# Kernel optimization log

Hardware: AMD Instinct MI355X
Metric: run time of the kernel (lower is better)

Reference implementation:

```python
import jax, jax.numpy as jnp
import numpy as np

IMG_W, IMG_H = 512, 512      # cfg.NETWORK.IMAGE_SIZE
HM_W, HM_H = 128, 128        # cfg.NETWORK.HEATMAP_SIZE
CUBE = (64, 64, 64)          # cube_size (voxel resolution)
N_VIEWS, BATCH, N_JOINTS = 5, 4, 15


def setup_inputs() -> dict:
    key = jax.random.key(0)
    k1, k2, k3 = jax.random.split(key, 3)
    heatmaps = jax.random.uniform(k1, (N_VIEWS, BATCH, N_JOINTS, HM_H, HM_W), jnp.float32)
    projM = jax.random.normal(k2, (N_VIEWS, BATCH, 3, 4), jnp.float32)
    grid_center = jax.random.normal(k3, (BATCH, 3), jnp.float32)
    return {"heatmaps": heatmaps, "projM": projM, "grid_center": grid_center, "grid_size": 8000}


def _compute_grid(grid_size, center):
    # torch.linspace(-s/2, s/2, n) + center[d], meshgrid 'ij' -> flattened [P, 3]
    half = jnp.float32(grid_size) * 0.5
    axes = [jnp.linspace(-half, half, n) + center[d] for d, n in enumerate(CUBE)]
    gx, gy, gz = jnp.meshgrid(*axes, indexing="ij")
    return jnp.stack([gx.ravel(), gy.ravel(), gz.ravel()], axis=-1)


def _bilinear(img, coords):
    # img: [J, H, W]; coords: [P, 2] normalized to [-1, 1], align_corners=True, zero padding
    J, H, W = img.shape
    ix = (coords[:, 0] + 1.0) * 0.5 * (W - 1)
    iy = (coords[:, 1] + 1.0) * 0.5 * (H - 1)
    x0 = jnp.floor(ix); y0 = jnp.floor(iy)
    x1 = x0 + 1.0;      y1 = y0 + 1.0
    wx1 = ix - x0; wx0 = 1.0 - wx1
    wy1 = iy - y0; wy0 = 1.0 - wy1

    def corner(xf, yf, w):
        valid = ((xf >= 0) & (xf <= W - 1) & (yf >= 0) & (yf <= H - 1)).astype(img.dtype)
        xi = jnp.clip(xf, 0, W - 1).astype(jnp.int32)
        yi = jnp.clip(yf, 0, H - 1).astype(jnp.int32)
        return img[:, yi, xi] * (w * valid)[None, :]  # [J, P]

    return (corner(x0, y0, wx0 * wy0) + corner(x1, y0, wx1 * wy0)
            + corner(x0, y1, wx0 * wy1) + corner(x1, y1, wx1 * wy1))


def reference(heatmaps, projM, grid_center, grid_size):
    n, B, J, H, W = heatmaps.shape
    dt = heatmaps.dtype
    # world-space voxel grids, one per batch sample: [B, P, 3]
    grids = jax.vmap(lambda c: _compute_grid(grid_size, c))(grid_center)
    P = grids.shape[1]
    # project_pose_sync takes grid with axes permuted [x, z, y]; pinhole 3x4 projection + perspective divide
    pts = grids[:, :, jnp.array([0, 2, 1])]
    homog = jnp.concatenate([pts, jnp.ones_like(pts[..., :1])], axis=-1)  # [B, P, 4]
    proj = jnp.einsum("nbij,bpj->nbpi", projM, homog)                     # [n, B, P, 3]
    xy = proj[..., :2] / proj[..., 2:3]                                   # [n, B, P, 2]
    # visibility mask per view
    inb = ((xy[..., 0] >= 0) & (xy[..., 1] >= 0)
           & (xy[..., 0] < IMG_W) & (xy[..., 1] < IMG_H)).astype(dt)      # [n, B, P]
    xy = jnp.clip(xy, -1.0, float(max(IMG_W, IMG_H)))
    xy = xy * jnp.array([HM_W / IMG_W, HM_H / IMG_H], dt)
    sg = jnp.clip(xy / jnp.array([HM_W - 1, HM_H - 1], dt) * 2.0 - 1.0, -1.1, 1.1)
    # bilinear grid_sample over all (view, batch) pairs at once
    samp = jax.vmap(_bilinear)(heatmaps.reshape(n * B, J, H, W),
                               sg.reshape(n * B, P, 2))                   # [n*B, J, P]
    samp = samp.reshape(n, B, J, P)
    num = jnp.einsum("nbjp,nbp->bjp", samp, inb)
    den = jnp.sum(inb, axis=0) + 1e-6                                     # [B, P]
    cubes = num / den[:, None, :]
    cubes = jnp.clip(jnp.where(jnp.isnan(cubes), 0.0, cubes), 0.0, 1.0)
    cubes = cubes.reshape(B, J, *CUBE)
    return cubes, grids
```

## Files before the change

### kernel.cpp

```cpp
#include <hip/hip_runtime.h>

#define NV 5
#define NB 4
#define NJ 15
#define HMW 128
#define HMH 128
#define P_TOTAL (64 * 64 * 64)
#define HM_PLANE (HMH * HMW)
#define CUBES_ELEMS ((size_t)NB * NJ * P_TOTAL)
#define N_PLANES (NV * NB * NJ)
#define QUAD_BYTES ((size_t)N_PLANES * HM_PLANE * 4)

typedef float f32x4 __attribute__((ext_vector_type(4)));
struct F2 { float x, y; };

__device__ __forceinline__ int dot4_i8(unsigned int a, unsigned int b, int c) {
#if __has_builtin(__builtin_amdgcn_sdot4)
    return __builtin_amdgcn_sdot4((int)a, (int)b, c, false);
#else
    return c + (int)(a & 0xff)         * (int)(b & 0xff)
             + (int)((a >> 8) & 0xff)  * (int)((b >> 8) & 0xff)
             + (int)((a >> 16) & 0xff) * (int)((b >> 16) & 0xff)
             + (int)((a >> 24) & 0xff) * (int)((b >> 24) & 0xff);
#endif
}

__global__ __launch_bounds__(256) void build_quads_i8(
    const float* __restrict__ hm, unsigned int* __restrict__ q)
{
    const int idx = blockIdx.x * 256 + threadIdx.x;
    const int qi  = idx & (HM_PLANE - 1);
    const int pl  = idx >> 14;
    const int within = qi & 15;
    const int tile   = qi >> 4;
    const int x = (tile & 31) * 4 + (within & 3);
    const int y = (tile >> 5) * 4 + (within >> 2);

    const float* img = hm + (size_t)pl * HM_PLANE;
    const int x1 = (x < 127) ? x + 1 : 127;
    const int y1 = (y < 127) ? y + 1 : 127;
    const unsigned int v00 = (unsigned int)(img[y  * HMW + x]  * 127.0f + 0.5f);
    const unsigned int v01 = (unsigned int)(img[y  * HMW + x1] * 127.0f + 0.5f);
    const unsigned int v10 = (unsigned int)(img[y1 * HMW + x]  * 127.0f + 0.5f);
    const unsigned int v11 = (unsigned int)(img[y1 * HMW + x1] * 127.0f + 0.5f);
    q[idx] = v00 | (v01 << 8) | (v10 << 16) | (v11 << 24);
}

__global__ __launch_bounds__(256) void project_layer_i8(
    const unsigned int* __restrict__ quads,
    const float* __restrict__ projM,
    const float* __restrict__ center,
    const int*   __restrict__ gsize,
    float* __restrict__ out)
{
    __shared__ float xpose[NJ + 3][256];

    const int blk = blockIdx.x;
    const int b   = blk >> 10;
    const int ib  = (blk >> 6) & 15;
    const int jb  = (blk >> 2) & 15;
    const int kb  = blk & 3;

    const int t  = threadIdx.x;
    const int w  = t >> 6;
    const int l  = t & 63;
    const int di = l >> 4;
    const int dj = (l >> 2) & 3;
    const int dk = l & 3;

    const int gi = ib * 4 + di;
    const int gj = jb * 4 + dj;
    const int gk = kb * 16 + w * 4 + dk;

    const float gs   = (float)gsize[0];
    const float half = gs * 0.5f;
    const float step = gs / 63.0f;

    const float cx = center[b * 3 + 0];
    const float cy = center[b * 3 + 1];
    const float cz = center[b * 3 + 2];

    const float gx = ((gi == 63) ? half : fmaf((float)gi, step, -half)) + cx;
    const float gy = ((gj == 63) ? half : fmaf((float)gj, step, -half)) + cy;
    const float gz = ((gk == 63) ? half : fmaf((float)gk, step, -half)) + cz;

    int num[NJ];
#pragma unroll
    for (int j = 0; j < NJ; ++j) num[j] = 0;
    int icnt = 0;

    for (int n = 0; n < NV; ++n) {
        const float* M = projM + ((size_t)(n * NB + b)) * 12;
        const float px = M[0] * gx + M[1] * gz + M[2]  * gy + M[3];
        const float py = M[4] * gx + M[5] * gz + M[6]  * gy + M[7];
        const float pz = M[8] * gx + M[9] * gz + M[10] * gy + M[11];

        const float rz = __builtin_amdgcn_rcpf(pz);
        const float u  = px * rz;
        const float v  = py * rz;

        const bool inb = (u >= 0.0f) && (v >= 0.0f) && (u < 512.0f) && (v < 512.0f);
        if (!inb) continue;

        icnt += 1;

        const float ix = u * 0.25f;
        const float iy = v * 0.25f;

        const float x0f = floorf(ix);
        const float y0f = floorf(iy);
        const float wx1 = ix - x0f, wx0 = 1.0f - wx1;
        const float wy1 = iy - y0f, wy0 = 1.0f - wy1;

        const int x0 = (int)x0f;
        const int y0 = (int)y0f;

        const float wx1v = (x0 < 127) ? wx1 : 0.0f;
        const float wy1v = (y0 < 127) ? wy1 : 0.0f;

        const unsigned int q00 = (unsigned int)(wx0  * wy0  * 127.0f + 0.5f);
        const unsigned int q01 = (unsigned int)(wx1v * wy0  * 127.0f + 0.5f);
        const unsigned int q10 = (unsigned int)(wx0  * wy1v * 127.0f + 0.5f);
        const unsigned int q11 = (unsigned int)(wx1v * wy1v * 127.0f + 0.5f);
        const unsigned int wpack = q00 | (q01 << 8) | (q10 << 16) | (q11 << 24);

        const int qidx = (((y0 >> 2) * 32 + (x0 >> 2)) << 4) | ((y0 & 3) << 2) | (x0 & 3);
        const unsigned int* qb = quads + (size_t)((n * NB + b) * NJ) * HM_PLANE + qidx;
#pragma unroll
        for (int j = 0; j < NJ; ++j) {
            const unsigned int qd = qb[(size_t)j * HM_PLANE];
            num[j] = dot4_i8(qd, wpack, num[j]);
        }
    }

    const float den = (float)icnt + 1e-6f;
    const float rs  = (1.0f / (127.0f * 127.0f)) / den;

    const int f = di * 64 + dj * 16 + w * 4 + dk;
    const int s = f ^ (((f >> 6) & 3) << 2);
#pragma unroll
    for (int j = 0; j < NJ; ++j)
        xpose[j][s] = fminf(fmaxf((float)num[j] * rs, 0.0f), 1.0f);
    xpose[NJ + 0][s] = gx;
    xpose[NJ + 1][s] = gy;
    xpose[NJ + 2][s] = gz;
    __syncthreads();

    for (int q = t; q < NJ * 64; q += 256) {
        const int j     = q >> 6;
        const int chunk = q & 63;
        const int i2 = chunk >> 4, j2 = (chunk >> 2) & 3, k4 = chunk & 3;
        const int fb = i2 * 64 + j2 * 16 + k4 * 4;
        const int sb = fb ^ (((fb >> 6) & 3) << 2);
        const f32x4 vals = *(const f32x4*)&xpose[j][sb];
        const size_t p = (size_t)(ib * 4 + i2) * 4096 + (jb * 4 + j2) * 64
                       + kb * 16 + k4 * 4;
        *(f32x4*)(out + (size_t)b * NJ * P_TOTAL + (size_t)j * P_TOTAL + p) = vals;
    }

    if (t < 192) {
        const int r  = t / 12;
        const int c4 = t - r * 12;
        const int i2 = r >> 2, j2 = r & 3;
        const int fb = i2 * 64 + j2 * 16;
        const size_t p0 = (size_t)(ib * 4 + i2) * 4096 + (jb * 4 + j2) * 64 + kb * 16;
        f32x4 v;
#pragma unroll
        for (int i = 0; i < 4; ++i) {
            const int idx  = c4 * 4 + i;
            const int pt   = idx / 3;
            const int comp = idx - pt * 3;
            const int ff = fb + pt;
            const int ss = ff ^ (((ff >> 6) & 3) << 2);
            v[i] = xpose[NJ + comp][ss];
        }
        *(f32x4*)(out + CUBES_ELEMS + ((size_t)b * P_TOTAL + p0) * 3 + c4 * 4) = v;
    }
}

__global__ __launch_bounds__(256) void project_layer_fallback(
    const float* __restrict__ hm,
    const float* __restrict__ projM,
    const float* __restrict__ center,
    const int*   __restrict__ gsize,
    float* __restrict__ out)
{
    const int blk = blockIdx.x;
    const int b   = blk >> 10;
    const int p   = ((blk & 1023) << 8) | threadIdx.x;
    const int gi  = p >> 12;
    const int gj  = (p >> 6) & 63;
    const int gk  = p & 63;

    const float gs   = (float)gsize[0];
    const float half = gs * 0.5f;
    const float step = gs / 63.0f;

    const float cx = center[b * 3 + 0];
    const float cy = center[b * 3 + 1];
    const float cz = center[b * 3 + 2];

    const float gx = ((gi == 63) ? half : fmaf((float)gi, step, -half)) + cx;
    const float gy = ((gj == 63) ? half : fmaf((float)gj, step, -half)) + cy;
    const float gz = ((gk == 63) ? half : fmaf((float)gk, step, -half)) + cz;

    float num[NJ];
#pragma unroll
    for (int j = 0; j < NJ; ++j) num[j] = 0.0f;
    float cnt = 0.0f;

    for (int n = 0; n < NV; ++n) {
        const float* M = projM + ((size_t)(n * NB + b)) * 12;
        const float px = M[0] * gx + M[1] * gz + M[2]  * gy + M[3];
        const float py = M[4] * gx + M[5] * gz + M[6]  * gy + M[7];
        const float pz = M[8] * gx + M[9] * gz + M[10] * gy + M[11];
        const float u = px / pz;
        const float v = py / pz;
        const bool inb = (u >= 0.0f) && (v >= 0.0f) && (u < 512.0f) && (v < 512.0f);
        if (!inb) continue;
        cnt += 1.0f;
        const float ix = u * 0.25f;
        const float iy = v * 0.25f;
        const float x0f = floorf(ix);
        const float y0f = floorf(iy);
        const float wx1 = ix - x0f, wx0 = 1.0f - wx1;
        const float wy1 = iy - y0f, wy0 = 1.0f - wy1;
        const int x0 = (int)x0f;
        const int y0 = (int)y0f;
        const bool  xe = (x0 == 127);
        const float wA = xe ? 0.0f : wx0;
        const float wB = xe ? wx0  : wx1;
        const float wy1v = (y0 <= 126) ? wy1 : 0.0f;
        const float wA0 = wA * wy0;
        const float wB0 = wB * wy0;
        const float wA1 = wA * wy1v;
        const float wB1 = wB * wy1v;
        const int xb  = xe ? 126 : x0;
        const int yr1 = (y0 <= 126) ? (y0 + 1) : 127;
        const int o0  = y0  * HMW + xb;
        const int o1  = yr1 * HMW + xb;
        const float* img = hm + ((size_t)(n * NB + b) * NJ) * HM_PLANE;
#pragma unroll
        for (int j = 0; j < NJ; ++j) {
            const float* ij = img + (size_t)j * HM_PLANE;
            const F2 r0 = *(const F2*)(ij + o0);
            const F2 r1 = *(const F2*)(ij + o1);
            num[j] += wA0 * r0.x + wB0 * r0.y + wA1 * r1.x + wB1 * r1.y;
        }
    }

    const float den = cnt + 1e-6f;
    {
        float* cb = out + (size_t)b * NJ * P_TOTAL + p;
#pragma unroll
        for (int j = 0; j < NJ; ++j) {
            const float c = num[j] / den;
            cb[(size_t)j * P_TOTAL] = fminf(fmaxf(c, 0.0f), 1.0f);
        }
    }
    {
        float* go = out + CUBES_ELEMS + ((size_t)b * P_TOTAL + p) * 3;
        go[0] = gx;
        go[1] = gy;
        go[2] = gz;
    }
}

extern "C" void kernel_launch(void* const* d_in, const int* in_sizes, int n_in,
                              void* d_out, int out_size, void* d_ws, size_t ws_size,
                              hipStream_t stream) {
    const float* hm     = (const float*)d_in[0];
    const float* projM  = (const float*)d_in[1];
    const float* center = (const float*)d_in[2];
    const int*   gsize  = (const int*)d_in[3];
    float* out = (float*)d_out;

    const int blocks = NB * 1024;

    if (ws_size >= QUAD_BYTES) {
        unsigned int* quads = (unsigned int*)d_ws;
        const int qthreads = N_PLANES * HM_PLANE;
        build_quads_i8<<<qthreads / 256, 256, 0, stream>>>(hm, quads);
        project_layer_i8<<<blocks, 256, 0, stream>>>(quads, projM, center, gsize, out);
    } else {
        project_layer_fallback<<<blocks, 256, 0, stream>>>(hm, projM, center, gsize, out);
    }
}
```

Before: 38.86 us.

## Process two adjacent z-voxels per thread and halve block count

Each thread now computes two neighbouring voxels along z. The x/y part of the projection is shared between them, and the loads for both gathers are issued together for more memory-level parallelism. The block count is halved, and the shared-memory transpose is written out in two half-passes with an extra barrier. This cuts per-voxel setup cost and launch overhead, in exchange for doubled accumulator registers (possible occupancy loss) and an extra sync.

```diff
diff --git a/kernel.cpp b/kernel.cpp
--- a/kernel.cpp
+++ b/kernel.cpp
@@ -46,7 +46,28 @@
     q[idx] = v00 | (v01 << 8) | (v10 << 16) | (v11 << 24);
 }
 
-__global__ __launch_bounds__(256) void project_layer_i8(
+__device__ __forceinline__ void sample_prep(
+    float u, float v, bool inb, unsigned int* wpack, int* qidx)
+{
+    const float ix = u * 0.25f;
+    const float iy = v * 0.25f;
+    const float x0f = floorf(ix);
+    const float y0f = floorf(iy);
+    const float wx1 = ix - x0f, wx0 = 1.0f - wx1;
+    const float wy1 = iy - y0f, wy0 = 1.0f - wy1;
+    const int x0 = (int)x0f;
+    const int y0 = (int)y0f;
+    const float wx1v = (x0 < 127) ? wx1 : 0.0f;
+    const float wy1v = (y0 < 127) ? wy1 : 0.0f;
+    const unsigned int q00 = (unsigned int)(wx0  * wy0  * 127.0f + 0.5f);
+    const unsigned int q01 = (unsigned int)(wx1v * wy0  * 127.0f + 0.5f);
+    const unsigned int q10 = (unsigned int)(wx0  * wy1v * 127.0f + 0.5f);
+    const unsigned int q11 = (unsigned int)(wx1v * wy1v * 127.0f + 0.5f);
+    *wpack = inb ? (q00 | (q01 << 8) | (q10 << 16) | (q11 << 24)) : 0u;
+    *qidx  = inb ? ((((y0 >> 2) * 32 + (x0 >> 2)) << 4) | ((y0 & 3) << 2) | (x0 & 3)) : 0;
+}
+
+__global__ __launch_bounds__(256) void project_layer_i8x2(
     const unsigned int* __restrict__ quads,
     const float* __restrict__ projM,
     const float* __restrict__ center,
@@ -56,10 +77,10 @@
     __shared__ float xpose[NJ + 3][256];
 
     const int blk = blockIdx.x;
-    const int b   = blk >> 10;
-    const int ib  = (blk >> 6) & 15;
-    const int jb  = (blk >> 2) & 15;
-    const int kb  = blk & 3;
+    const int b   = blk >> 9;
+    const int ib  = (blk >> 5) & 15;
+    const int jb  = (blk >> 1) & 15;
+    const int kb  = blk & 1;
 
     const int t  = threadIdx.x;
     const int w  = t >> 6;
@@ -68,9 +89,11 @@
     const int dj = (l >> 2) & 3;
     const int dk = l & 3;
 
-    const int gi = ib * 4 + di;
-    const int gj = jb * 4 + dj;
-    const int gk = kb * 16 + w * 4 + dk;
+    const int gi  = ib * 4 + di;
+    const int gj  = jb * 4 + dj;
+    const int kpA = w * 8 + dk * 2;
+    const int gkA = kb * 32 + kpA;
+    const int gkB = gkA + 1;
 
     const float gs   = (float)gsize[0];
     const float half = gs * 0.5f;
@@ -80,101 +103,111 @@
     const float cy = center[b * 3 + 1];
     const float cz = center[b * 3 + 2];
 
-    const float gx = ((gi == 63) ? half : fmaf((float)gi, step, -half)) + cx;
-    const float gy = ((gj == 63) ? half : fmaf((float)gj, step, -half)) + cy;
-    const float gz = ((gk == 63) ? half : fmaf((float)gk, step, -half)) + cz;
-
-    int num[NJ];
-#pragma unroll
-    for (int j = 0; j < NJ; ++j) num[j] = 0;
-    int icnt = 0;
+    const float gx  = ((gi  == 63) ? half : fmaf((float)gi,  step, -half)) + cx;
+    const float gy  = ((gj  == 63) ? half : fmaf((float)gj,  step, -half)) + cy;
+    const float gzA = ((gkA == 63) ? half : fmaf((float)gkA, step, -half)) + cz;
+    const float gzB = ((gkB == 63) ? half : fmaf((float)gkB, step, -half)) + cz;
+
+    int numA[NJ], numB[NJ];
+#pragma unroll
+    for (int j = 0; j < NJ; ++j) { numA[j] = 0; numB[j] = 0; }
+    int icntA = 0, icntB = 0;
 
     for (int n = 0; n < NV; ++n) {
         const float* M = projM + ((size_t)(n * NB + b)) * 12;
-        const float px = M[0] * gx + M[1] * gz + M[2]  * gy + M[3];
-        const float py = M[4] * gx + M[5] * gz + M[6]  * gy + M[7];
-        const float pz = M[8] * gx + M[9] * gz + M[10] * gy + M[11];
-
-        const float rz = __builtin_amdgcn_rcpf(pz);
-        const float u  = px * rz;
-        const float v  = py * rz;
-
-        const bool inb = (u >= 0.0f) && (v >= 0.0f) && (u < 512.0f) && (v < 512.0f);
-        if (!inb) continue;
-
-        icnt += 1;
-
-        const float ix = u * 0.25f;
-        const float iy = v * 0.25f;
-
-        const float x0f = floorf(ix);
-        const float y0f = floorf(iy);
-        const float wx1 = ix - x0f, wx0 = 1.0f - wx1;
-        const float wy1 = iy - y0f, wy0 = 1.0f - wy1;
-
-        const int x0 = (int)x0f;
-        const int y0 = (int)y0f;
-
-        const float wx1v = (x0 < 127) ? wx1 : 0.0f;
-        const float wy1v = (y0 < 127) ? wy1 : 0.0f;
-
-        const unsigned int q00 = (unsigned int)(wx0  * wy0  * 127.0f + 0.5f);
-        const unsigned int q01 = (unsigned int)(wx1v * wy0  * 127.0f + 0.5f);
-        const unsigned int q10 = (unsigned int)(wx0  * wy1v * 127.0f + 0.5f);
-        const unsigned int q11 = (unsigned int)(wx1v * wy1v * 127.0f + 0.5f);
-        const unsigned int wpack = q00 | (q01 << 8) | (q10 << 16) | (q11 << 24);
-
-        const int qidx = (((y0 >> 2) * 32 + (x0 >> 2)) << 4) | ((y0 & 3) << 2) | (x0 & 3);
-        const unsigned int* qb = quads + (size_t)((n * NB + b) * NJ) * HM_PLANE + qidx;
+        const float pxc = M[0] * gx + M[2]  * gy + M[3];
+        const float pyc = M[4] * gx + M[6]  * gy + M[7];
+        const float pzc = M[8] * gx + M[10] * gy + M[11];
+
+        const float pxA = pxc + M[1] * gzA, pxB = pxc + M[1] * gzB;
+        const float pyA = pyc + M[5] * gzA, pyB = pyc + M[5] * gzB;
+        const float pzA = pzc + M[9] * gzA, pzB = pzc + M[9] * gzB;
+
+        const float rzA = __builtin_amdgcn_rcpf(pzA);
+        const float rzB = __builtin_amdgcn_rcpf(pzB);
+        const float uA = pxA * rzA, vA = pyA * rzA;
+        const float uB = pxB * rzB, vB = pyB * rzB;
+
+        const bool inbA = (uA >= 0.0f) && (vA >= 0.0f) && (uA < 512.0f) && (vA < 512.0f);
+        const bool inbB = (uB >= 0.0f) && (vB >= 0.0f) && (uB < 512.0f) && (vB < 512.0f);
+        if (!inbA && !inbB) continue;
+
+        icntA += inbA ? 1 : 0;
+        icntB += inbB ? 1 : 0;
+
+        unsigned int wpA, wpB;
+        int qiA, qiB;
+        sample_prep(uA, vA, inbA, &wpA, &qiA);
+        sample_prep(uB, vB, inbB, &wpB, &qiB);
+        if (!inbA) qiA = qiB;
+        if (!inbB) qiB = qiA;
+
+        const unsigned int* qp = quads + (size_t)((n * NB + b) * NJ) * HM_PLANE;
+        const unsigned int* qbA = qp + qiA;
+        const unsigned int* qbB = qp + qiB;
 #pragma unroll
         for (int j = 0; j < NJ; ++j) {
-            const unsigned int qd = qb[(size_t)j * HM_PLANE];
-            num[j] = dot4_i8(qd, wpack, num[j]);
-        }
-    }
-
-    const float den = (float)icnt + 1e-6f;
-    const float rs  = (1.0f / (127.0f * 127.0f)) / den;
-
-    const int f = di * 64 + dj * 16 + w * 4 + dk;
-    const int s = f ^ (((f >> 6) & 3) << 2);
-#pragma unroll
-    for (int j = 0; j < NJ; ++j)
-        xpose[j][s] = fminf(fmaxf((float)num[j] * rs, 0.0f), 1.0f);
-    xpose[NJ + 0][s] = gx;
-    xpose[NJ + 1][s] = gy;
-    xpose[NJ + 2][s] = gz;
-    __syncthreads();
-
-    for (int q = t; q < NJ * 64; q += 256) {
-        const int j     = q >> 6;
-        const int chunk = q & 63;
-        const int i2 = chunk >> 4, j2 = (chunk >> 2) & 3, k4 = chunk & 3;
-        const int fb = i2 * 64 + j2 * 16 + k4 * 4;
-        const int sb = fb ^ (((fb >> 6) & 3) << 2);
-        const f32x4 vals = *(const f32x4*)&xpose[j][sb];
-        const size_t p = (size_t)(ib * 4 + i2) * 4096 + (jb * 4 + j2) * 64
-                       + kb * 16 + k4 * 4;
-        *(f32x4*)(out + (size_t)b * NJ * P_TOTAL + (size_t)j * P_TOTAL + p) = vals;
-    }
-
-    if (t < 192) {
-        const int r  = t / 12;
-        const int c4 = t - r * 12;
-        const int i2 = r >> 2, j2 = r & 3;
-        const int fb = i2 * 64 + j2 * 16;
-        const size_t p0 = (size_t)(ib * 4 + i2) * 4096 + (jb * 4 + j2) * 64 + kb * 16;
-        f32x4 v;
-#pragma unroll
-        for (int i = 0; i < 4; ++i) {
-            const int idx  = c4 * 4 + i;
-            const int pt   = idx / 3;
-            const int comp = idx - pt * 3;
-            const int ff = fb + pt;
-            const int ss = ff ^ (((ff >> 6) & 3) << 2);
-            v[i] = xpose[NJ + comp][ss];
-        }
-        *(f32x4*)(out + CUBES_ELEMS + ((size_t)b * P_TOTAL + p0) * 3 + c4 * 4) = v;
+            const unsigned int qdA = qbA[(size_t)j * HM_PLANE];
+            const unsigned int qdB = qbB[(size_t)j * HM_PLANE];
+            numA[j] = dot4_i8(qdA, wpA, numA[j]);
+            numB[j] = dot4_i8(qdB, wpB, numB[j]);
+        }
+    }
+
+    const float rsA = (1.0f / (127.0f * 127.0f)) / ((float)icntA + 1e-6f);
+    const float rsB = (1.0f / (127.0f * 127.0f)) / ((float)icntB + 1e-6f);
+
+    const int fA = di * 64 + dj * 16 + (kpA & 15);
+    const int sA = fA ^ (((fA >> 6) & 3) << 2);
+    const int myHalf = w >> 1;
+
+#pragma unroll
+    for (int h = 0; h < 2; ++h) {
+        if (h) __syncthreads();
+        if (myHalf == h) {
+#pragma unroll
+            for (int j = 0; j < NJ; ++j) {
+                xpose[j][sA]     = fminf(fmaxf((float)numA[j] * rsA, 0.0f), 1.0f);
+                xpose[j][sA + 1] = fminf(fmaxf((float)numB[j] * rsB, 0.0f), 1.0f);
+            }
+            xpose[NJ + 0][sA] = gx;  xpose[NJ + 0][sA + 1] = gx;
+            xpose[NJ + 1][sA] = gy;  xpose[NJ + 1][sA + 1] = gy;
+            xpose[NJ + 2][sA] = gzA; xpose[NJ + 2][sA + 1] = gzB;
+        }
+        __syncthreads();
+
+        const int kbase = kb * 32 + h * 16;
+
+        for (int q = t; q < NJ * 64; q += 256) {
+            const int j     = q >> 6;
+            const int chunk = q & 63;
+            const int i2 = chunk >> 4, j2 = (chunk >> 2) & 3, k4 = chunk & 3;
+            const int fb = i2 * 64 + j2 * 16 + k4 * 4;
+            const int sb = fb ^ (((fb >> 6) & 3) << 2);
+            const f32x4 vals = *(const f32x4*)&xpose[j][sb];
+            const size_t p = (size_t)(ib * 4 + i2) * 4096 + (jb * 4 + j2) * 64
+                           + kbase + k4 * 4;
+            *(f32x4*)(out + (size_t)b * NJ * P_TOTAL + (size_t)j * P_TOTAL + p) = vals;
+        }
+
+        if (t < 192) {
+            const int r  = t / 12;
+            const int c4 = t - r * 12;
+            const int i2 = r >> 2, j2 = r & 3;
+            const int fb = i2 * 64 + j2 * 16;
+            const size_t p0 = (size_t)(ib * 4 + i2) * 4096 + (jb * 4 + j2) * 64 + kbase;
+            f32x4 v;
+#pragma unroll
+            for (int i = 0; i < 4; ++i) {
+                const int idx  = c4 * 4 + i;
+                const int pt   = idx / 3;
+                const int comp = idx - pt * 3;
+                const int ff = fb + pt;
+                const int ss = ff ^ (((ff >> 6) & 3) << 2);
+                v[i] = xpose[NJ + comp][ss];
+            }
+            *(f32x4*)(out + CUBES_ELEMS + ((size_t)b * P_TOTAL + p0) * 3 + c4 * 4) = v;
+        }
     }
 }
 
@@ -275,14 +308,12 @@
     const int*   gsize  = (const int*)d_in[3];
     float* out = (float*)d_out;
 
-    const int blocks = NB * 1024;
-
     if (ws_size >= QUAD_BYTES) {
         unsigned int* quads = (unsigned int*)d_ws;
         const int qthreads = N_PLANES * HM_PLANE;
         build_quads_i8<<<qthreads / 256, 256, 0, stream>>>(hm, quads);
-        project_layer_i8<<<blocks, 256, 0, stream>>>(quads, projM, center, gsize, out);
+        project_layer_i8x2<<<NB * 512, 256, 0, stream>>>(quads, projM, center, gsize, out);
     } else {
-        project_layer_fallback<<<blocks, 256, 0, stream>>>(hm, projM, center, gsize, out);
-    }
-}
+        project_layer_fallback<<<NB * 1024, 256, 0, stream>>>(hm, projM, center, gsize, out);
+    }
+}
```

Measured after the change: 63.85 us. 1.64x slower.

## Vectorize quad-build kernel and scramble projection block order

Applied to the files above, without the earlier changes.

The heatmap-to-int8-quad packing kernel now has each thread load two float4 rows plus edge elements and write four packed quads with one 128-bit store, instead of doing four scalar loads per output quad. This cuts the thread count by four and removes the redundant scalar gathers. The projection kernel also remaps blockIdx with an odd multiplier mod 4096. That spreads concurrently running blocks across different batches and spatial regions, which may improve cache or channel balance but could also hurt locality.

```diff
diff --git a/kernel.cpp b/kernel.cpp
--- a/kernel.cpp
+++ b/kernel.cpp
@@ -12,6 +12,7 @@
 #define QUAD_BYTES ((size_t)N_PLANES * HM_PLANE * 4)
 
 typedef float f32x4 __attribute__((ext_vector_type(4)));
+typedef unsigned int u32x4 __attribute__((ext_vector_type(4)));
 struct F2 { float x, y; };
 
 __device__ __forceinline__ int dot4_i8(unsigned int a, unsigned int b, int c) {
@@ -25,25 +26,40 @@
 #endif
 }
 
-__global__ __launch_bounds__(256) void build_quads_i8(
+__device__ __forceinline__ unsigned int q7(float v) {
+    return (unsigned int)(v * 127.0f + 0.5f);
+}
+
+__global__ __launch_bounds__(256) void build_quads_i8v2(
     const float* __restrict__ hm, unsigned int* __restrict__ q)
 {
-    const int idx = blockIdx.x * 256 + threadIdx.x;
-    const int qi  = idx & (HM_PLANE - 1);
-    const int pl  = idx >> 14;
-    const int within = qi & 15;
-    const int tile   = qi >> 4;
-    const int x = (tile & 31) * 4 + (within & 3);
-    const int y = (tile >> 5) * 4 + (within >> 2);
+    const int idx  = blockIdx.x * 256 + threadIdx.x;
+    const int unit = idx & 4095;
+    const int pl   = idx >> 12;
+    const int trow = unit & 3;
+    const int tile = unit >> 2;
+    const int tx   = tile & 31;
+    const int ty   = tile >> 5;
+    const int x0   = tx * 4;
+    const int y    = ty * 4 + trow;
+    const int y1   = (y < 127) ? y + 1 : 127;
 
     const float* img = hm + (size_t)pl * HM_PLANE;
-    const int x1 = (x < 127) ? x + 1 : 127;
-    const int y1 = (y < 127) ? y + 1 : 127;
-    const unsigned int v00 = (unsigned int)(img[y  * HMW + x]  * 127.0f + 0.5f);
-    const unsigned int v01 = (unsigned int)(img[y  * HMW + x1] * 127.0f + 0.5f);
-    const unsigned int v10 = (unsigned int)(img[y1 * HMW + x]  * 127.0f + 0.5f);
-    const unsigned int v11 = (unsigned int)(img[y1 * HMW + x1] * 127.0f + 0.5f);
-    q[idx] = v00 | (v01 << 8) | (v10 << 16) | (v11 << 24);
+    const f32x4 r0 = *(const f32x4*)(img + y  * HMW + x0);
+    const f32x4 r1 = *(const f32x4*)(img + y1 * HMW + x0);
+    const float e0 = (x0 + 4 < 128) ? img[y  * HMW + x0 + 4] : r0[3];
+    const float e1 = (x0 + 4 < 128) ? img[y1 * HMW + x0 + 4] : r1[3];
+
+    u32x4 o;
+#pragma unroll
+    for (int wx = 0; wx < 4; ++wx) {
+        const float v00 = r0[wx];
+        const float v01 = (wx < 3) ? r0[wx + 1] : e0;
+        const float v10 = r1[wx];
+        const float v11 = (wx < 3) ? r1[wx + 1] : e1;
+        o[wx] = q7(v00) | (q7(v01) << 8) | (q7(v10) << 16) | (q7(v11) << 24);
+    }
+    *(u32x4*)(q + ((size_t)pl << 14) + ((size_t)tile << 4) + (trow << 2)) = o;
 }
 
 __global__ __launch_bounds__(256) void project_layer_i8(
@@ -55,7 +71,7 @@
 {
     __shared__ float xpose[NJ + 3][256];
 
-    const int blk = blockIdx.x;
+    const int blk = (blockIdx.x * 2469) & 4095;
     const int b   = blk >> 10;
     const int ib  = (blk >> 6) & 15;
     const int jb  = (blk >> 2) & 15;
@@ -118,10 +134,10 @@
         const float wx1v = (x0 < 127) ? wx1 : 0.0f;
         const float wy1v = (y0 < 127) ? wy1 : 0.0f;
 
-        const unsigned int q00 = (unsigned int)(wx0  * wy0  * 127.0f + 0.5f);
-        const unsigned int q01 = (unsigned int)(wx1v * wy0  * 127.0f + 0.5f);
-        const unsigned int q10 = (unsigned int)(wx0  * wy1v * 127.0f + 0.5f);
-        const unsigned int q11 = (unsigned int)(wx1v * wy1v * 127.0f + 0.5f);
+        const unsigned int q00 = q7(wx0  * wy0 );
+        const unsigned int q01 = q7(wx1v * wy0 );
+        const unsigned int q10 = q7(wx0  * wy1v);
+        const unsigned int q11 = q7(wx1v * wy1v);
         const unsigned int wpack = q00 | (q01 << 8) | (q10 << 16) | (q11 << 24);
 
         const int qidx = (((y0 >> 2) * 32 + (x0 >> 2)) << 4) | ((y0 & 3) << 2) | (x0 & 3);
@@ -275,14 +291,12 @@
     const int*   gsize  = (const int*)d_in[3];
     float* out = (float*)d_out;
 
-    const int blocks = NB * 1024;
-
     if (ws_size >= QUAD_BYTES) {
         unsigned int* quads = (unsigned int*)d_ws;
-        const int qthreads = N_PLANES * HM_PLANE;
-        build_quads_i8<<<qthreads / 256, 256, 0, stream>>>(hm, quads);
-        project_layer_i8<<<blocks, 256, 0, stream>>>(quads, projM, center, gsize, out);
+        const int qunits = N_PLANES * 4096;
+        build_quads_i8v2<<<qunits / 256, 256, 0, stream>>>(hm, quads);
+        project_layer_i8<<<NB * 1024, 256, 0, stream>>>(quads, projM, center, gsize, out);
     } else {
-        project_layer_fallback<<<blocks, 256, 0, stream>>>(hm, projM, center, gsize, out);
-    }
-}
+        project_layer_fallback<<<NB * 1024, 256, 0, stream>>>(hm, projM, center, gsize, out);
+    }
+}
```

After: 34.17 us (median of 2 runs). -12.1%, faster.
